# Kernel optimization log

Hardware: AMD Instinct MI355X
Metric: run time of the kernel (lower is better)

## Reference

```python
import jax, jax.numpy as jnp
import numpy as np

WS = 7          # window size (fixed: last_idx=169=(2*7-1)^2)
NP = 1          # num_priorset
NH = 8          # num heads
DIM = 256
SHIFT = 3
N = WS * WS     # 49 tokens per window
NK = N + 3 * NP # 52 K/V tokens (window + uk/fg/bg priors)


def _rel_index():
    coords = np.stack(np.meshgrid(np.arange(WS), np.arange(WS), indexing='ij')).reshape(2, -1)
    rel = (coords[:, :, None] - coords[:, None, :]).transpose(1, 2, 0).astype(np.int64)
    rel[:, :, 0] += WS - 1
    rel[:, :, 1] += WS - 1
    rel[:, :, 0] *= 2 * WS - 1
    idx = rel.sum(-1)                      # (49,49) in [0,168]
    full = np.full((N, NK), 169, dtype=np.int64)
    full[:, :N] = idx
    for j in range(3 * NP):
        full[:, N + j] = 169 + j           # dedicated bias rows for priors
    return jnp.asarray(full)

REL_IDX = _rel_index()


def _ln(t, g, b, eps=1e-5):
    mu = t.mean(-1, keepdims=True)
    var = ((t - mu) ** 2).mean(-1, keepdims=True)
    return (t - mu) * jax.lax.rsqrt(var + eps) * g + b


def setup_inputs() -> dict:
    key = jax.random.key(0)
    ks = jax.random.split(key, 16)
    B, H, W, C = 4, 112, 112, DIM
    nW = (H // WS) * (W // WS)
    hid = 4 * C
    inp = {
        'x': jax.random.normal(ks[0], (B, H * W, C), jnp.float32),
        'mask_matrix': jax.random.normal(ks[1], (nW, N, N), jnp.float32),
        'area_fg': jax.random.uniform(ks[2], (B, H, W, 1), jnp.float32),
        'area_bg': jax.random.uniform(ks[3], (B, H, W, 1), jnp.float32),
        'area_uk': jax.random.uniform(ks[4], (B, H, W, 1), jnp.float32),
        'norm1_g': jnp.ones((C,), jnp.float32),
        'norm1_b': jnp.zeros((C,), jnp.float32),
        'norm2_g': jnp.ones((C,), jnp.float32),
        'norm2_b': jnp.zeros((C,), jnp.float32),
        'qkv_w': jax.random.normal(ks[5], (3 * C, C), jnp.float32) * 0.02,
        'qkv_b': jnp.zeros((3 * C,), jnp.float32),
        'proj_w': jax.random.normal(ks[6], (C, C), jnp.float32) * 0.02,
        'proj_b': jnp.zeros((C,), jnp.float32),
        'rel_table': jax.random.normal(ks[7], (169 + 3 * NP, NH), jnp.float32) * 0.02,
        'fc1_w': jax.random.normal(ks[8], (hid, C), jnp.float32) * 0.02,
        'fc1_b': jnp.zeros((hid,), jnp.float32),
        'fc2_w': jax.random.normal(ks[9], (C, hid), jnp.float32) * 0.02,
        'fc2_b': jnp.zeros((C,), jnp.float32),
        'H': 112,
        'W': 112,
    }
    return inp


def reference(x, mask_matrix, area_fg, area_bg, area_uk,
              norm1_g, norm1_b, norm2_g, norm2_b,
              qkv_w, qkv_b, proj_w, proj_b, rel_table,
              fc1_w, fc1_b, fc2_w, fc2_b, H, W):
    B, L, C = x.shape
    d = C // NH
    scale = d ** -0.5
    nWh, nWw = H // WS, W // WS
    nW = nWh * nWw

    shortcut = x
    x4 = x.reshape(B, H, W, C)
    eps = 1e-9
    # masked global-average prior tokens (B, C)
    def pooled(area):
        return (area * x4).sum((1, 2)) / (area.sum((1, 2)) + eps)
    uk, fg, bg = pooled(area_uk), pooled(area_fg), pooled(area_bg)

    xn = _ln(x, norm1_g, norm1_b).reshape(B, H, W, C)
    uk_n = _ln(uk, norm1_g, norm1_b)
    fg_n = _ln(fg, norm1_g, norm1_b)
    bg_n = _ln(bg, norm1_g, norm1_b)

    # cyclic shift + window partition (H,W divisible by WS -> no padding)
    xs = jnp.roll(xn, (-SHIFT, -SHIFT), (1, 2))
    xw = xs.reshape(B, nWh, WS, nWw, WS, C).transpose(0, 1, 3, 2, 4, 5).reshape(B * nW, N, C)

    # prior highway tokens (order: unknown, fg, bg) and per-window copies
    ph = jnp.stack([uk_n, fg_n, bg_n], axis=1)                      # (B,3,C)
    pr = jnp.broadcast_to(ph[:, None], (B, nW, 3, C)).reshape(B * nW, 3, C)
    xk = jnp.concatenate([xw, pr], axis=1)                          # (B_,52,C)

    qkv = (xk @ qkv_w.T + qkv_b).reshape(B * nW, NK, 3, NH, d)
    q = qkv[:, :N, 0].transpose(0, 2, 1, 3) * scale                 # (B_,h,49,d)
    k = qkv[:, :, 1].transpose(0, 2, 1, 3)                          # (B_,h,52,d)
    v = qkv[:, :, 2].transpose(0, 2, 1, 3)

    attn = jnp.einsum('bhnd,bhmd->bhnm', q, k)                      # (B_,h,49,52)
    bias = rel_table[REL_IDX].transpose(2, 0, 1)                    # (h,49,52)
    attn = attn + bias[None]
    mask = jnp.pad(mask_matrix, ((0, 0), (0, 0), (0, 3 * NP)))      # (nW,49,52)
    attn = attn.reshape(B, nW, NH, N, NK) + mask[None, :, None]
    attn = jax.nn.softmax(attn.reshape(B * nW, NH, N, NK), axis=-1)

    out = jnp.einsum('bhnm,bhmd->bhnd', attn, v)
    out = out.transpose(0, 2, 1, 3).reshape(B * nW, N, C)
    out = out @ proj_w.T + proj_b

    # prior highway: qkv on priors, keep V, project
    ph_qkv = (ph @ qkv_w.T + qkv_b).reshape(B, 3 * NP, 3, NH, d)
    v_hw = ph_qkv[:, :, 2].reshape(B, 3 * NP, C) @ proj_w.T + proj_b

    # window reverse + reverse shift
    xo = out.reshape(B, nWh, nWw, WS, WS, C).transpose(0, 1, 3, 2, 4, 5).reshape(B, H, W, C)
    xo = jnp.roll(xo, (SHIFT, SHIFT), (1, 2)).reshape(B, L, C)

    x = shortcut + xo
    h = _ln(x, norm2_g, norm2_b)
    h = jax.nn.gelu(h @ fc1_w.T + fc1_b, approximate=False)
    x = x + (h @ fc2_w.T + fc2_b)
    return x, v_hw
```

## Files before the change

kernel.cpp:

```cpp
#include <hip/hip_runtime.h>
#include <hip/hip_bf16.h>
#include <math.h>

typedef __bf16 bf16;
typedef bf16 bf16x8 __attribute__((ext_vector_type(8)));
typedef bf16 bf16x4 __attribute__((ext_vector_type(4)));
typedef float f32x4 __attribute__((ext_vector_type(4)));

constexpr int DIM   = 256;
constexpr int NH    = 8;
constexpr int LTOT  = 112 * 112;
constexpr int BTOT  = 4;
constexpr int MROWS = BTOT * LTOT;
constexpr int MQKV  = MROWS + BTOT * 3;
constexpr int NTOK  = 49;
constexpr int NKV   = 52;

__global__ __launch_bounds__(256) void cvt_all(
    const float* __restrict__ qkvw, const float* __restrict__ projw,
    const float* __restrict__ fc1w, const float* __restrict__ fc2w,
    bf16* __restrict__ d)
{
    int i = blockIdx.x * 256 + threadIdx.x;
    float v;
    if (i < 196608)      v = qkvw[i];
    else if (i < 262144) v = projw[i - 196608];
    else if (i < 524288) v = fc1w[i - 262144];
    else                 v = fc2w[i - 524288];
    d[i] = (bf16)v;
}

__global__ __launch_bounds__(256) void pool_partial(
    const float* __restrict__ x, const float* __restrict__ afg,
    const float* __restrict__ abg, const float* __restrict__ auk,
    float* __restrict__ pnum, float* __restrict__ pden)
{
    int b = blockIdx.x / 196, ch = blockIdx.x % 196;
    int p0 = ch * 64, tid = threadIdx.x;
    __shared__ float su[64], sf[64], sb[64];
    if (tid < 64) {
        int p = p0 + tid;
        su[tid] = auk[b * LTOT + p];
        sf[tid] = afg[b * LTOT + p];
        sb[tid] = abg[b * LTOT + p];
    }
    __syncthreads();
    float nu = 0.f, nf = 0.f, nb = 0.f;
    const float* xp = x + ((size_t)b * LTOT + p0) * DIM + tid;
    for (int pp = 0; pp < 64; ++pp) {
        float xv = xp[(size_t)pp * DIM];
        nu += su[pp] * xv; nf += sf[pp] * xv; nb += sb[pp] * xv;
    }
    size_t base = (size_t)blockIdx.x * 3 * DIM + tid;
    pnum[base]           = nu;
    pnum[base + DIM]     = nf;
    pnum[base + 2 * DIM] = nb;
    if (tid < 3) {
        const float* sptr = tid == 0 ? su : (tid == 1 ? sf : sb);
        float t = 0.f;
        for (int i = 0; i < 64; ++i) t += sptr[i];
        pden[blockIdx.x * 3 + tid] = t;
    }
}

__device__ __forceinline__ void block_meanvar(float v, float& mu, float& rstd, float eps) {
    float s = v, s2 = v * v;
    #pragma unroll
    for (int o = 32; o >= 1; o >>= 1) { s += __shfl_down(s, o); s2 += __shfl_down(s2, o); }
    __shared__ float ps[4], ps2[4];
    int w = threadIdx.x >> 6, ln = threadIdx.x & 63;
    if (ln == 0) { ps[w] = s; ps2[w] = s2; }
    __syncthreads();
    float S  = ps[0] + ps[1] + ps[2] + ps[3];
    float S2 = ps2[0] + ps2[1] + ps2[2] + ps2[3];
    mu = S * (1.f / 256.f);
    float var = S2 * (1.f / 256.f) - mu * mu;
    rstd = rsqrtf(var + eps);
}

__global__ __launch_bounds__(256) void prior_ln(
    const float* __restrict__ pnum, const float* __restrict__ pden,
    const float* __restrict__ g, const float* __restrict__ bt, bf16* __restrict__ xn)
{
    int b = blockIdx.x / 3, j = blockIdx.x % 3, tid = threadIdx.x;
    float s = 0.f, den = 0.f;
    for (int ch = 0; ch < 196; ++ch) {
        s   += pnum[((size_t)(b * 196 + ch) * 3 + j) * DIM + tid];
        den += pden[(b * 196 + ch) * 3 + j];
    }
    float v = s / (den + 1e-9f);
    float mu, rs;
    block_meanvar(v, mu, rs, 1e-5f);
    xn[((size_t)MROWS + blockIdx.x) * DIM + tid] = (bf16)((v - mu) * rs * g[tid] + bt[tid]);
}

__global__ __launch_bounds__(512) void ln1_kernel(
    const float* __restrict__ x, const float* __restrict__ g,
    const float* __restrict__ bt, bf16* __restrict__ xn)
{
    const size_t row = (size_t)blockIdx.x * 8 + (threadIdx.x >> 6);
    const int lane = threadIdx.x & 63;
    f32x4 v = *(const f32x4*)(x + row * DIM + lane * 4);
    float s  = v[0] + v[1] + v[2] + v[3];
    float s2 = v[0]*v[0] + v[1]*v[1] + v[2]*v[2] + v[3]*v[3];
    #pragma unroll
    for (int o = 32; o >= 1; o >>= 1) { s += __shfl_xor(s, o); s2 += __shfl_xor(s2, o); }
    float mu = s * (1.f / 256.f);
    float var = s2 * (1.f / 256.f) - mu * mu;
    float rs = rsqrtf(var + 1e-5f);
    f32x4 gv = *(const f32x4*)(g + lane * 4);
    f32x4 bv = *(const f32x4*)(bt + lane * 4);
    bf16x4 o;
    #pragma unroll
    for (int u = 0; u < 4; ++u) o[u] = (bf16)((v[u] - mu) * rs * gv[u] + bv[u]);
    *(bf16x4*)(xn + row * DIM + lane * 4) = o;
}

__device__ __forceinline__ void load_lds16(const void* g, void* l) {
    __builtin_amdgcn_global_load_lds((const __attribute__((address_space(1))) void*)g,
                                     (__attribute__((address_space(3))) void*)l, 16, 0, 0);
}

template <int EPI, int K, int N>
__global__ __launch_bounds__(256) void gemm_bt(
    const bf16* __restrict__ A, const bf16* __restrict__ W,
    const float* __restrict__ bias, bf16* __restrict__ Cb,
    float* __restrict__ Cf, const float* __restrict__ resid, int M)
{
    __shared__ __align__(16) char smem[49152];
    const int tid = threadIdx.x;
    const int wv = tid >> 6, lane = tid & 63;

    const int gx = gridDim.x;
    const int nwg = gx * (int)gridDim.y;
    int lin = blockIdx.y * gx + blockIdx.x;
    int xcd = lin & 7, loc = lin >> 3;
    int qq = nwg >> 3, rr = nwg & 7;
    int nid = (xcd < rr ? xcd * (qq + 1) : rr * (qq + 1) + (xcd - rr) * qq) + loc;
    int by = nid / gx, bx = nid - by * gx;
    const int m0 = by * 128, n0 = bx * 128;

    const int r  = tid >> 2;
    const int kb = (((tid & 3) ^ ((tid >> 3) & 3)) * 8);
    const int wr = (wv >> 1) * 64, wc = (wv & 1) * 64;
    const int fr = lane & 15;
    const int fo = (((lane >> 4) ^ ((fr >> 1) & 3)) * 8);

    int ra0 = m0 + r;      if (ra0 >= M) ra0 = M - 1;
    int ra1 = m0 + r + 64; if (ra1 >= M) ra1 = M - 1;
    const bf16* pA0 = A + (size_t)ra0 * K + kb;
    const bf16* pA1 = A + (size_t)ra1 * K + kb;
    const bf16* pW0 = W + (size_t)(n0 + r) * K + kb;
    const bf16* pW1 = W + (size_t)(n0 + r + 64) * K + kb;

    const f32x4 zero = {0.f, 0.f, 0.f, 0.f};
    f32x4 acc[4][4];
    #pragma unroll
    for (int i = 0; i < 4; ++i)
        #pragma unroll
        for (int j = 0; j < 4; ++j) acc[i][j] = zero;

    constexpr int nK = K >> 5;

    auto stage = [&](int kt, int b) {
        bf16* Ab = (bf16*)(smem + b * 16384);
        bf16* Bb = (bf16*)(smem + b * 16384 + 8192);
        const int off = kt * 32;
        load_lds16(pA0 + off, Ab + wv * 512);
        load_lds16(pA1 + off, Ab + 2048 + wv * 512);
        load_lds16(pW0 + off, Bb + wv * 512);
        load_lds16(pW1 + off, Bb + 2048 + wv * 512);
    };

    stage(0, 0);
    stage(1, 1);

    #pragma unroll
    for (int kt = 0; kt < nK; ++kt) {
        const int cur = kt % 3;
        asm volatile("s_waitcnt lgkmcnt(0)" ::: "memory");
        if (kt < nK - 1) asm volatile("s_waitcnt vmcnt(4)" ::: "memory");
        else             asm volatile("s_waitcnt vmcnt(0)" ::: "memory");
        __builtin_amdgcn_s_barrier();
        if (kt + 2 < nK) stage(kt + 2, (kt + 2) % 3);
        const bf16* Ac = (const bf16*)(smem + cur * 16384);
        const bf16* Bc = (const bf16*)(smem + cur * 16384 + 8192);
        bf16x8 af[4], bw[4];
        #pragma unroll
        for (int i = 0; i < 4; ++i) af[i] = *(const bf16x8*)(Ac + (wr + i * 16 + fr) * 32 + fo);
        #pragma unroll
        for (int i = 0; i < 4; ++i) bw[i] = *(const bf16x8*)(Bc + (wc + i * 16 + fr) * 32 + fo);
        #pragma unroll
        for (int i = 0; i < 4; ++i)
            #pragma unroll
            for (int j = 0; j < 4; ++j)
                acc[i][j] = __builtin_amdgcn_mfma_f32_16x16x32_bf16(af[i], bw[j], acc[i][j], 0, 0, 0);
    }
    __syncthreads();

    const int cr = (lane >> 4) * 4, cc = lane & 15;
    if constexpr (EPI == 3) {
        float* Cs = (float*)smem;
        #pragma unroll
        for (int half = 0; half < 2; ++half) {
            if (wr == half * 64) {
                #pragma unroll
                for (int i = 0; i < 4; ++i)
                    #pragma unroll
                    for (int j = 0; j < 4; ++j) {
                        const int col = wc + j * 16 + cc;
                        const float bv = bias[n0 + col];
                        #pragma unroll
                        for (int q = 0; q < 4; ++q)
                            Cs[(i * 16 + cr + q) * 132 + col] = acc[i][j][q] + bv;
                    }
            }
            __syncthreads();
            for (int p = tid; p < 2048; p += 256) {
                const int row = p >> 5, seg = (p & 31) * 4;
                const int gr = m0 + half * 64 + row;
                if (gr < M) {
                    f32x4 v = *(const f32x4*)(Cs + row * 132 + seg);
                    const size_t o = (size_t)gr * N + n0 + seg;
                    f32x4 rv = *(const f32x4*)(resid + o);
                    *(f32x4*)(Cf + o) = v + rv;
                }
            }
            __syncthreads();
        }
    } else {
        bf16* Csb = (bf16*)smem;
        #pragma unroll
        for (int i = 0; i < 4; ++i)
            #pragma unroll
            for (int j = 0; j < 4; ++j) {
                const int col = wc + j * 16 + cc;
                const float bv = bias[n0 + col];
                #pragma unroll
                for (int q = 0; q < 4; ++q) {
                    float v = acc[i][j][q] + bv;
                    if constexpr (EPI == 2) {
                        float u = 0.7978845608028654f * (v + 0.044715f * v * v * v);
                        v = v / (1.f + __expf(-2.f * u));
                    }
                    Csb[(wr + i * 16 + cr + q) * 144 + col] = (bf16)v;
                }
            }
        __syncthreads();
        for (int p = tid; p < 2048; p += 256) {
            const int row = p >> 4, seg = (p & 15) * 8;
            const int gr = m0 + row;
            if (gr < M)
                *(bf16x8*)(Cb + (size_t)gr * N + n0 + seg) = *(const bf16x8*)(Csb + row * 144 + seg);
        }
    }
}

__global__ __launch_bounds__(256) void proj_ln2(
    const bf16* __restrict__ A, const bf16* __restrict__ W,
    const float* __restrict__ bias, const float* __restrict__ x,
    const float* __restrict__ g, const float* __restrict__ bt,
    float* __restrict__ x2, bf16* __restrict__ ln2)
{
    __shared__ __align__(16) char smem[40960];
    bf16* As = (bf16*)smem;
    bf16* Bs = (bf16*)(smem + 8192);

    const int tid = threadIdx.x;
    const int wv = tid >> 6, lane = tid & 63;
    const int m0 = blockIdx.x * 64;

    const int r4 = tid >> 2;
    const int kb = (((tid & 3) ^ ((tid >> 3) & 3)) * 8);
    const int fr = lane & 15;
    const int fo = (((lane >> 4) ^ ((fr >> 1) & 3)) * 8);

    const bf16* pA  = A + (size_t)(m0 + r4) * 256 + kb;
    const bf16* pW0 = W + (size_t)(r4)       * 256 + kb;
    const bf16* pW1 = W + (size_t)(r4 + 64)  * 256 + kb;
    const bf16* pW2 = W + (size_t)(r4 + 128) * 256 + kb;
    const bf16* pW3 = W + (size_t)(r4 + 192) * 256 + kb;

    const f32x4 zero = {0.f, 0.f, 0.f, 0.f};
    f32x4 acc[4][4];
    #pragma unroll
    for (int i = 0; i < 4; ++i)
        #pragma unroll
        for (int j = 0; j < 4; ++j) acc[i][j] = zero;

    auto stage = [&](int kt, int b) {
        const int off = kt * 32;
        load_lds16(pA  + off, As + b * 2048 + wv * 512);
        load_lds16(pW0 + off, Bs + b * 8192 + wv * 512);
        load_lds16(pW1 + off, Bs + b * 8192 + 2048 + wv * 512);
        load_lds16(pW2 + off, Bs + b * 8192 + 4096 + wv * 512);
        load_lds16(pW3 + off, Bs + b * 8192 + 6144 + wv * 512);
    };

    stage(0, 0);
    __syncthreads();
    #pragma unroll
    for (int kt = 0; kt < 8; ++kt) {
        const int cur = kt & 1;
        if (kt + 1 < 8) stage(kt + 1, cur ^ 1);
        const bf16* Ac = As + cur * 2048;
        const bf16* Bc = Bs + cur * 8192;
        bf16x8 af[4], bw[4];
        #pragma unroll
        for (int i = 0; i < 4; ++i) af[i] = *(const bf16x8*)(Ac + (i * 16 + fr) * 32 + fo);
        #pragma unroll
        for (int j = 0; j < 4; ++j) bw[j] = *(const bf16x8*)(Bc + (wv * 64 + j * 16 + fr) * 32 + fo);
        #pragma unroll
        for (int i = 0; i < 4; ++i)
            #pragma unroll
            for (int j = 0; j < 4; ++j)
                acc[i][j] = __builtin_amdgcn_mfma_f32_16x16x32_bf16(af[i], bw[j], acc[i][j], 0, 0, 0);
        __syncthreads();
    }

    float* red = (float*)smem;
    const int cr = (lane >> 4) * 4, cc = lane & 15;

    int nrw[4][4];
    #pragma unroll
    for (int i = 0; i < 4; ++i)
        #pragma unroll
        for (int q = 0; q < 4; ++q) {
            int ar = m0 + i * 16 + cr + q;
            int bwin = ar / 49;
            int n = ar - bwin * 49;
            int bb = bwin >> 8, w = bwin & 255;
            int ni = n / 7, nj = n - ni * 7;
            int hh = (w >> 4) * 7 + ni + 3;  if (hh >= 112) hh -= 112;
            int ww2 = (w & 15) * 7 + nj + 3; if (ww2 >= 112) ww2 -= 112;
            nrw[i][q] = bb * LTOT + hh * 112 + ww2;
        }

    float s1[4][4], s2[4][4];
    #pragma unroll
    for (int i = 0; i < 4; ++i)
        #pragma unroll
        for (int q = 0; q < 4; ++q) { s1[i][q] = 0.f; s2[i][q] = 0.f; }

    #pragma unroll
    for (int j = 0; j < 4; ++j) {
        const int col = wv * 64 + j * 16 + cc;
        const float bv = bias[col];
        #pragma unroll
        for (int i = 0; i < 4; ++i)
            #pragma unroll
            for (int q = 0; q < 4; ++q) {
                float v = acc[i][j][q] + bv + x[(size_t)nrw[i][q] * 256 + col];
                acc[i][j][q] = v;
                s1[i][q] += v; s2[i][q] += v * v;
            }
    }
    #pragma unroll
    for (int o = 1; o < 16; o <<= 1)
        #pragma unroll
        for (int i = 0; i < 4; ++i)
            #pragma unroll
            for (int q = 0; q < 4; ++q) {
                s1[i][q] += __shfl_xor(s1[i][q], o);
                s2[i][q] += __shfl_xor(s2[i][q], o);
            }
    if (cc == 0) {
        #pragma unroll
        for (int i = 0; i < 4; ++i)
            #pragma unroll
            for (int q = 0; q < 4; ++q) {
                int m = i * 16 + cr + q;
                red[m * 8 + wv * 2]     = s1[i][q];
                red[m * 8 + wv * 2 + 1] = s2[i][q];
            }
    }
    __syncthreads();

    float mu[4][4], rs[4][4];
    #pragma unroll
    for (int i = 0; i < 4; ++i)
        #pragma unroll
        for (int q = 0; q < 4; ++q) {
            int m = i * 16 + cr + q;
            float S  = red[m * 8] + red[m * 8 + 2] + red[m * 8 + 4] + red[m * 8 + 6];
            float S2 = red[m * 8 + 1] + red[m * 8 + 3] + red[m * 8 + 5] + red[m * 8 + 7];
            float mm = S * (1.f / 256.f);
            float var = S2 * (1.f / 256.f) - mm * mm;
            mu[i][q] = mm;
            rs[i][q] = rsqrtf(var + 1e-5f);
        }
    #pragma unroll
    for (int j = 0; j < 4; ++j) {
        const int col = wv * 64 + j * 16 + cc;
        const float gv = g[col], bv2 = bt[col];
        #pragma unroll
        for (int i = 0; i < 4; ++i)
            #pragma unroll
            for (int q = 0; q < 4; ++q) {
                float v = acc[i][j][q];
                size_t o = (size_t)nrw[i][q] * 256 + col;
                x2[o] = v;
                ln2[o] = (bf16)((v - mu[i][q]) * rs[i][q] * gv + bv2);
            }
    }
}

__global__ __launch_bounds__(512, 1) void attn_kernel(
    const bf16* __restrict__ qkv, const float* __restrict__ mask,
    const float* __restrict__ rel, bf16* __restrict__ att_out)
{
    __shared__ int rowtab[52];
    __shared__ float mLds[64 * 67];
    __shared__ float rLds[1376];
    __shared__ __align__(16) bf16 vT[8 * 32 * 80];
    __shared__ __align__(16) bf16 pbuf[8 * 64 * 80];

    const int tid = threadIdx.x;
    const int bw = blockIdx.x;
    const int b = bw >> 8, w = bw & 255;
    const int wh = w >> 4, wwi = w & 15;

    if (tid < 52) {
        int row;
        if (tid < 49) {
            int i = tid / 7, j = tid % 7;
            int gh = wh * 7 + i + 3;  if (gh >= 112) gh -= 112;
            int gw = wwi * 7 + j + 3; if (gw >= 112) gw -= 112;
            row = b * LTOT + gh * 112 + gw;
        } else {
            row = MROWS + b * 3 + (tid - 49);
        }
        rowtab[tid] = row;
    }
    __syncthreads();

    for (int e = tid; e < 64 * 67; e += 512) {
        int q = e / 67, k = e % 67;
        mLds[e] = (q < 49 && k < 49) ? mask[(size_t)w * 2401 + q * 49 + k] : 0.f;
    }
    for (int e = tid; e < 1376; e += 512) rLds[e] = rel[e];
    for (int e = tid; e < 256 * 12; e += 512) {
        int rr = e / 12, c = 52 + e % 12;
        vT[rr * 80 + c] = (bf16)0.f;
    }
    for (int e = tid; e < 52 * 256; e += 512) {
        int key = e >> 8, c = e & 255;
        vT[c * 80 + key] = qkv[(size_t)rowtab[key] * 768 + 512 + c];
    }
    __syncthreads();

    const int h    = tid >> 6;
    const int lane = tid & 63;
    const int cl   = lane & 15;
    const int hi4  = lane >> 4;
    const int cr   = hi4 * 4;
    const int fo   = hi4 * 8;

    bf16x8 kf[4], qf[4];
    #pragma unroll
    for (int i = 0; i < 4; ++i) {
        int key = 16 * i + cl; if (key > 51) key = 51;
        kf[i] = *(const bf16x8*)(qkv + (size_t)rowtab[key] * 768 + 256 + h * 32 + fo);
    }
    #pragma unroll
    for (int j = 0; j < 4; ++j) {
        int qq = 16 * j + cl; if (qq > 48) qq = 48;
        qf[j] = *(const bf16x8*)(qkv + (size_t)rowtab[qq] * 768 + h * 32 + fo);
    }
    const f32x4 zero = {0.f, 0.f, 0.f, 0.f};
    f32x4 acc[4][4];
    #pragma unroll
    for (int i = 0; i < 4; ++i)
        #pragma unroll
        for (int j = 0; j < 4; ++j) acc[i][j] = zero;
    #pragma unroll
    for (int i = 0; i < 4; ++i)
        #pragma unroll
        for (int j = 0; j < 4; ++j)
            acc[i][j] = __builtin_amdgcn_mfma_f32_16x16x32_bf16(kf[i], qf[j], acc[i][j], 0, 0, 0);

    int kb[4][4];
    #pragma unroll
    for (int i = 0; i < 4; ++i)
        #pragma unroll
        for (int r = 0; r < 4; ++r) {
            int key = 16 * i + cr + r;
            kb[i][r] = (key / 7) * 13 + (key % 7);
        }
    bf16* pW = pbuf + h * (64 * 80);
    #pragma unroll
    for (int j = 0; j < 4; ++j) {
        const int q = 16 * j + cl;
        const int i1 = q / 7, j1 = q % 7;
        const int qb = (i1 + 6) * 13 + (j1 + 6);
        float sv[16];
        float mx = -3e38f;
        #pragma unroll
        for (int i = 0; i < 4; ++i)
            #pragma unroll
            for (int r = 0; r < 4; ++r) {
                int key = 16 * i + cr + r;
                int idx = key < 49 ? (qb - kb[i][r]) : (169 + key - 49);
                idx = idx < 0 ? 0 : (idx > 171 ? 171 : idx);
                float s = acc[i][j][r] * 0.17677669529663687f
                        + mLds[q * 67 + key] + rLds[idx * 8 + h];
                if (key >= 52) s = -3e38f;
                sv[i * 4 + r] = s;
                mx = fmaxf(mx, s);
            }
        mx = fmaxf(mx, __shfl_xor(mx, 16));
        mx = fmaxf(mx, __shfl_xor(mx, 32));
        float sum = 0.f;
        #pragma unroll
        for (int e = 0; e < 16; ++e) { float p = __expf(sv[e] - mx); sv[e] = p; sum += p; }
        sum += __shfl_xor(sum, 16);
        sum += __shfl_xor(sum, 32);
        const float inv = 1.f / sum;
        #pragma unroll
        for (int i = 0; i < 4; ++i) {
            bf16x4 pk;
            #pragma unroll
            for (int r = 0; r < 4; ++r) pk[r] = (bf16)(sv[i * 4 + r] * inv);
            *(bf16x4*)(pW + q * 80 + 16 * i + cr) = pk;
        }
    }

    f32x4 oacc[4][2];
    #pragma unroll
    for (int i = 0; i < 4; ++i) { oacc[i][0] = zero; oacc[i][1] = zero; }
    #pragma unroll
    for (int ks = 0; ks < 2; ++ks) {
        bf16x8 vf[2];
        #pragma unroll
        for (int j2 = 0; j2 < 2; ++j2)
            vf[j2] = *(const bf16x8*)(vT + (h * 32 + 16 * j2 + cl) * 80 + 32 * ks + fo);
        #pragma unroll
        for (int i = 0; i < 4; ++i) {
            bf16x8 pf = *(const bf16x8*)(pW + (16 * i + cl) * 80 + 32 * ks + fo);
            #pragma unroll
            for (int j2 = 0; j2 < 2; ++j2)
                oacc[i][j2] = __builtin_amdgcn_mfma_f32_16x16x32_bf16(pf, vf[j2], oacc[i][j2], 0, 0, 0);
        }
    }

    #pragma unroll
    for (int i = 0; i < 4; ++i)
        #pragma unroll
        for (int r = 0; r < 4; ++r) {
            int q = 16 * i + cr + r;
            if (q < 49) {
                bf16* op = att_out + ((size_t)bw * 49 + q) * 256 + h * 32 + cl;
                op[0]  = (bf16)oacc[i][0][r];
                op[16] = (bf16)oacc[i][1][r];
            }
        }
}

__global__ __launch_bounds__(256) void vhw_kernel(
    const bf16* __restrict__ qkv, const float* __restrict__ pw,
    const float* __restrict__ pb, float* __restrict__ outp)
{
    int rowI = blockIdx.x;
    int c = threadIdx.x;
    const bf16* vp = qkv + (size_t)(MROWS + rowI) * 768 + 512;
    const float* wr_ = pw + (size_t)c * DIM;
    float acc = pb[c];
    for (int k = 0; k < DIM; ++k) acc += (float)vp[k] * wr_[k];
    outp[(size_t)rowI * DIM + c] = acc;
}

extern "C" void kernel_launch(void* const* d_in, const int* in_sizes, int n_in,
                              void* d_out, int out_size, void* d_ws, size_t ws_size,
                              hipStream_t stream)
{
    const float* x     = (const float*)d_in[0];
    const float* mask  = (const float*)d_in[1];
    const float* afg   = (const float*)d_in[2];
    const float* abg   = (const float*)d_in[3];
    const float* auk   = (const float*)d_in[4];
    const float* n1g   = (const float*)d_in[5];
    const float* n1b   = (const float*)d_in[6];
    const float* n2g   = (const float*)d_in[7];
    const float* n2b   = (const float*)d_in[8];
    const float* qkvw  = (const float*)d_in[9];
    const float* qkvb  = (const float*)d_in[10];
    const float* projw = (const float*)d_in[11];
    const float* projb = (const float*)d_in[12];
    const float* rel   = (const float*)d_in[13];
    const float* fc1w  = (const float*)d_in[14];
    const float* fc1b  = (const float*)d_in[15];
    const float* fc2w  = (const float*)d_in[16];
    const float* fc2b  = (const float*)d_in[17];
    float* out = (float*)d_out;
    char*  ws  = (char*)d_ws;

    bf16*  wq   = (bf16*)(ws + 0);
    bf16*  wp   = (bf16*)(ws + 393216);
    bf16*  wf1  = (bf16*)(ws + 524288);
    bf16*  wf2  = (bf16*)(ws + 1048576);
    float* pnum = (float*)(ws + (28ull << 20));
    float* pden = (float*)(ws + (28ull << 20) + 2408448);
    bf16* xn    = (bf16*)(ws + (2ull << 20));
    bf16* atto  = (bf16*)(ws + (2ull << 20));
    bf16* hbuf  = (bf16*)(ws + (2ull << 20));
    bf16* qkvo  = (bf16*)(ws + (28ull << 20));
    bf16* ln2b  = (bf16*)(ws + (102ull << 20));

    cvt_all<<<3072, 256, 0, stream>>>(qkvw, projw, fc1w, fc2w, (bf16*)ws);

    pool_partial<<<BTOT * 196, 256, 0, stream>>>(x, afg, abg, auk, pnum, pden);
    prior_ln<<<12, 256, 0, stream>>>(pnum, pden, n1g, n1b, xn);
    ln1_kernel<<<MROWS / 8, 512, 0, stream>>>(x, n1g, n1b, xn);

    gemm_bt<0, 256, 768><<<dim3(6, 393), 256, 0, stream>>>(xn, wq, qkvb, qkvo, nullptr, nullptr, MQKV);

    attn_kernel<<<BTOT * 256, 512, 0, stream>>>(qkvo, mask, rel, atto);
    vhw_kernel<<<12, 256, 0, stream>>>(qkvo, projw, projb, out + (size_t)MROWS * DIM);

    proj_ln2<<<MROWS / 64, 256, 0, stream>>>(atto, wp, projb, x, n2g, n2b, out, ln2b);

    gemm_bt<2, 256, 1024><<<dim3(8, 392), 256, 0, stream>>>(ln2b, wf1, fc1b, hbuf, nullptr, nullptr, MROWS);

    gemm_bt<3, 1024, 256><<<dim3(2, 392), 256, 0, stream>>>(hbuf, wf2, fc2b, nullptr, out, out, MROWS);

    (void)in_sizes; (void)n_in; (void)out_size; (void)ws_size;
}
```

Before: 305.5 us.

## Stage proj GEMM tile in LDS for coalesced residual+LayerNorm epilogue; add MFMA priority hints

The proj GEMM epilogue now writes the bias-added accumulator tile into shared memory in two halves. Each wave then processes whole rows: it does a vectorized float4 gather of the residual x, computes the LayerNorm with a single wave-wide shuffle reduction, and writes x2 and ln2 with contiguous vector stores. The goal is to replace the scattered per-element 16-lane-wide accesses and the cross-wave reduction through LDS. The attention kernel also wraps its MFMA loops in s_setprio hints. The cost is extra LDS traffic and barriers in the epilogue.

```diff
diff --git a/kernel.cpp b/kernel.cpp
--- a/kernel.cpp
+++ b/kernel.cpp
@@ -318,90 +318,52 @@
         __syncthreads();
     }
 
-    float* red = (float*)smem;
+    float* Cs = (float*)smem;
     const int cr = (lane >> 4) * 4, cc = lane & 15;
-
-    int nrw[4][4];
-    #pragma unroll
-    for (int i = 0; i < 4; ++i)
-        #pragma unroll
-        for (int q = 0; q < 4; ++q) {
-            int ar = m0 + i * 16 + cr + q;
+    const f32x4 gv  = *(const f32x4*)(g  + lane * 4);
+    const f32x4 bv2 = *(const f32x4*)(bt + lane * 4);
+    #pragma unroll
+    for (int h = 0; h < 2; ++h) {
+        #pragma unroll
+        for (int i2 = 0; i2 < 2; ++i2) {
+            const int i = h * 2 + i2;
+            #pragma unroll
+            for (int j = 0; j < 4; ++j) {
+                const int col = wv * 64 + j * 16 + cc;
+                const float bv = bias[col];
+                #pragma unroll
+                for (int q = 0; q < 4; ++q)
+                    Cs[(i2 * 16 + cr + q) * 260 + col] = acc[i][j][q] + bv;
+            }
+        }
+        __syncthreads();
+        #pragma unroll
+        for (int it = 0; it < 8; ++it) {
+            const int rl = wv * 8 + it;
+            const int ar = m0 + h * 32 + rl;
             int bwin = ar / 49;
             int n = ar - bwin * 49;
             int bb = bwin >> 8, w = bwin & 255;
             int ni = n / 7, nj = n - ni * 7;
             int hh = (w >> 4) * 7 + ni + 3;  if (hh >= 112) hh -= 112;
             int ww2 = (w & 15) * 7 + nj + 3; if (ww2 >= 112) ww2 -= 112;
-            nrw[i][q] = bb * LTOT + hh * 112 + ww2;
-        }
-
-    float s1[4][4], s2[4][4];
-    #pragma unroll
-    for (int i = 0; i < 4; ++i)
-        #pragma unroll
-        for (int q = 0; q < 4; ++q) { s1[i][q] = 0.f; s2[i][q] = 0.f; }
-
-    #pragma unroll
-    for (int j = 0; j < 4; ++j) {
-        const int col = wv * 64 + j * 16 + cc;
-        const float bv = bias[col];
-        #pragma unroll
-        for (int i = 0; i < 4; ++i)
-            #pragma unroll
-            for (int q = 0; q < 4; ++q) {
-                float v = acc[i][j][q] + bv + x[(size_t)nrw[i][q] * 256 + col];
-                acc[i][j][q] = v;
-                s1[i][q] += v; s2[i][q] += v * v;
-            }
-    }
-    #pragma unroll
-    for (int o = 1; o < 16; o <<= 1)
-        #pragma unroll
-        for (int i = 0; i < 4; ++i)
-            #pragma unroll
-            for (int q = 0; q < 4; ++q) {
-                s1[i][q] += __shfl_xor(s1[i][q], o);
-                s2[i][q] += __shfl_xor(s2[i][q], o);
-            }
-    if (cc == 0) {
-        #pragma unroll
-        for (int i = 0; i < 4; ++i)
-            #pragma unroll
-            for (int q = 0; q < 4; ++q) {
-                int m = i * 16 + cr + q;
-                red[m * 8 + wv * 2]     = s1[i][q];
-                red[m * 8 + wv * 2 + 1] = s2[i][q];
-            }
-    }
-    __syncthreads();
-
-    float mu[4][4], rs[4][4];
-    #pragma unroll
-    for (int i = 0; i < 4; ++i)
-        #pragma unroll
-        for (int q = 0; q < 4; ++q) {
-            int m = i * 16 + cr + q;
-            float S  = red[m * 8] + red[m * 8 + 2] + red[m * 8 + 4] + red[m * 8 + 6];
-            float S2 = red[m * 8 + 1] + red[m * 8 + 3] + red[m * 8 + 5] + red[m * 8 + 7];
-            float mm = S * (1.f / 256.f);
-            float var = S2 * (1.f / 256.f) - mm * mm;
-            mu[i][q] = mm;
-            rs[i][q] = rsqrtf(var + 1e-5f);
-        }
-    #pragma unroll
-    for (int j = 0; j < 4; ++j) {
-        const int col = wv * 64 + j * 16 + cc;
-        const float gv = g[col], bv2 = bt[col];
-        #pragma unroll
-        for (int i = 0; i < 4; ++i)
-            #pragma unroll
-            for (int q = 0; q < 4; ++q) {
-                float v = acc[i][j][q];
-                size_t o = (size_t)nrw[i][q] * 256 + col;
-                x2[o] = v;
-                ln2[o] = (bf16)((v - mu[i][q]) * rs[i][q] * gv + bv2);
-            }
+            const size_t nrow = (size_t)(bb * LTOT + hh * 112 + ww2);
+            f32x4 pv = *(const f32x4*)(Cs + rl * 260 + lane * 4);
+            f32x4 xv = *(const f32x4*)(x + nrow * 256 + lane * 4);
+            f32x4 v = pv + xv;
+            float s1 = v[0] + v[1] + v[2] + v[3];
+            float s2 = v[0]*v[0] + v[1]*v[1] + v[2]*v[2] + v[3]*v[3];
+            #pragma unroll
+            for (int o = 32; o >= 1; o >>= 1) { s1 += __shfl_xor(s1, o); s2 += __shfl_xor(s2, o); }
+            float mu = s1 * (1.f / 256.f);
+            float rs = rsqrtf(s2 * (1.f / 256.f) - mu * mu + 1e-5f);
+            *(f32x4*)(x2 + nrow * 256 + lane * 4) = v;
+            bf16x4 ov;
+            #pragma unroll
+            for (int u = 0; u < 4; ++u) ov[u] = (bf16)((v[u] - mu) * rs * gv[u] + bv2[u]);
+            *(bf16x4*)(ln2 + nrow * 256 + lane * 4) = ov;
+        }
+        __syncthreads();
     }
 }
 
@@ -473,11 +435,13 @@
     for (int i = 0; i < 4; ++i)
         #pragma unroll
         for (int j = 0; j < 4; ++j) acc[i][j] = zero;
+    __builtin_amdgcn_s_setprio(1);
     #pragma unroll
     for (int i = 0; i < 4; ++i)
         #pragma unroll
         for (int j = 0; j < 4; ++j)
             acc[i][j] = __builtin_amdgcn_mfma_f32_16x16x32_bf16(kf[i], qf[j], acc[i][j], 0, 0, 0);
+    __builtin_amdgcn_s_setprio(0);
 
     int kb[4][4];
     #pragma unroll
@@ -534,6 +498,7 @@
         #pragma unroll
         for (int j2 = 0; j2 < 2; ++j2)
             vf[j2] = *(const bf16x8*)(vT + (h * 32 + 16 * j2 + cl) * 80 + 32 * ks + fo);
+        __builtin_amdgcn_s_setprio(1);
         #pragma unroll
         for (int i = 0; i < 4; ++i) {
             bf16x8 pf = *(const bf16x8*)(pW + (16 * i + cl) * 80 + 32 * ks + fo);
@@ -541,6 +506,7 @@
             for (int j2 = 0; j2 < 2; ++j2)
                 oacc[i][j2] = __builtin_amdgcn_mfma_f32_16x16x32_bf16(pf, vf[j2], oacc[i][j2], 0, 0, 0);
         }
+        __builtin_amdgcn_s_setprio(0);
     }
 
     #pragma unroll
```

Result: faster. 295.9 us (-3.1%).
